# Kernel optimization log

Measured on AMD Instinct MI355X. Metric: run time of the kernel, lower is better.

## Reference

```python
import jax, jax.numpy as jnp
import numpy as np

H = 1024
NH = 16
HD = H // NH
EPS = 1e-5


def setup_inputs() -> dict:
    key = jax.random.key(0)
    ks = jax.random.split(key, 16)
    B, LQ, LK = 2, 1024, 2048
    s = 1.0 / np.sqrt(H)
    inp = {
        "query": jax.random.normal(ks[0], (B, LQ, H), jnp.float32),
        "key": jax.random.normal(ks[1], (B, LK, H), jnp.float32),
        "value": jax.random.normal(ks[2], (B, LK, H), jnp.float32),
        "mask": jax.random.randint(ks[3], (B, LQ, LK), 0, 2, jnp.int32),
        "Wq": jax.random.normal(ks[4], (H, H), jnp.float32) * s,
        "bq": jnp.zeros((H,), jnp.float32),
        "Wk": jax.random.normal(ks[5], (H, H), jnp.float32) * s,
        "bk": jnp.zeros((H,), jnp.float32),
        "Wv": jax.random.normal(ks[6], (H, H), jnp.float32) * s,
        "bv": jnp.zeros((H,), jnp.float32),
        "Wo": jax.random.normal(ks[7], (H, H), jnp.float32) * s,
        "bo": jnp.zeros((H,), jnp.float32),
        "ln_g": jnp.ones((H,), jnp.float32),
        "ln_b": jnp.zeros((H,), jnp.float32),
    }
    return inp


def _split_heads(x, B, L):
    # [B, L, H] -> [B, NH, L, HD]
    return x.reshape(B, L, NH, HD).transpose(0, 2, 1, 3)


def reference(query, key, value, mask, Wq, bq, Wk, bk, Wv, bv, Wo, bo, ln_g, ln_b):
    B, LQ, _ = query.shape
    LK = key.shape[1]
    # projections (torch Linear: x @ W.T + b)
    Q = _split_heads(query @ Wq.T + bq, B, LQ)   # [B,NH,LQ,HD]
    K = _split_heads(key   @ Wk.T + bk, B, LK)   # [B,NH,LK,HD]
    V = _split_heads(value @ Wv.T + bv, B, LK)   # [B,NH,LK,HD]
    scores = jnp.einsum('bhqd,bhkd->bhqk', Q, K) / np.sqrt(HD)
    scores = jnp.where(mask[:, None, :, :] == 0, jnp.float32(-1e9), scores)
    attn = jax.nn.softmax(scores, axis=-1)
    # dropout is identity in eval mode
    ctx = jnp.einsum('bhqk,bhkd->bhqd', attn, V)            # [B,NH,LQ,HD]
    ctx = ctx.transpose(0, 2, 1, 3).reshape(B, LQ, H)       # [B,LQ,H]
    out = ctx @ Wo.T + bo
    x = out + query
    mu = jnp.mean(x, axis=-1, keepdims=True)
    var = jnp.mean(jnp.square(x - mu), axis=-1, keepdims=True)
    return (x - mu) / jnp.sqrt(var + EPS) * ln_g + ln_b
```

## Files before the change

kernel.cpp:

```cpp
#include <hip/hip_runtime.h>
#include <hip/hip_bf16.h>

typedef __hip_bfloat16 hbf16;

#define Hdim 1024
#define NHEAD 16
#define HDIM 64
#define BATCH 2
#define LQ 1024
#define LK 2048
#define LN_EPS 1e-5f

typedef __bf16 bfv8 __attribute__((ext_vector_type(8)));
typedef float floatx4 __attribute__((ext_vector_type(4)));
typedef union { bfv8 v; __bf16 b[8]; unsigned short s[8]; } bfu8;

#define BK 32
#define LDS_PITCH 40
#define QT 64
#define KT 64
#define KS_PITCH 72
#define VT_OFF(d) ((d) * 72 + (((d) >> 3) << 3))
#define PS_OFF(r) ((r) * 72 + (((r) >> 2) << 3))

__device__ inline bfv8 cvt2(const float4 x, const float4 y) {
    bfv8 r = {(__bf16)x.x, (__bf16)x.y, (__bf16)x.z, (__bf16)x.w,
              (__bf16)y.x, (__bf16)y.y, (__bf16)y.z, (__bf16)y.w};
    return r;
}

__device__ __forceinline__ void glds16(const void* g, void* l) {
    __builtin_amdgcn_global_load_lds(
        (const __attribute__((address_space(1))) void*)g,
        (__attribute__((address_space(3))) void*)l, 16, 0, 0);
}

__global__ __launch_bounds__(256) void cvt_all(
    const float* __restrict__ q, const float* __restrict__ k,
    const float* __restrict__ v, const float* __restrict__ Wq,
    const float* __restrict__ Wk, const float* __restrict__ Wv,
    hbf16* __restrict__ qb, hbf16* __restrict__ kb, hbf16* __restrict__ vb,
    hbf16* __restrict__ Wqb, hbf16* __restrict__ Wkb, hbf16* __restrict__ Wvb) {
    const int blk = blockIdx.x;
    const float* src; hbf16* dst; int base;
    if (blk < 1024)      { src = q;  dst = qb;  base = blk; }
    else if (blk < 3072) { src = k;  dst = kb;  base = blk - 1024; }
    else if (blk < 5120) { src = v;  dst = vb;  base = blk - 3072; }
    else if (blk < 5632) { src = Wq; dst = Wqb; base = blk - 5120; }
    else if (blk < 6144) { src = Wk; dst = Wkb; base = blk - 5632; }
    else                 { src = Wv; dst = Wvb; base = blk - 6144; }
    const size_t e = (size_t)base * 2048 + (size_t)threadIdx.x * 8;
    const float4 a = *(const float4*)(src + e);
    const float4 b = *(const float4*)(src + e + 4);
    *(bfv8*)((__bf16*)dst + e) = cvt2(a, b);
}

__global__ __launch_bounds__(256) void proj3_glds(
    const hbf16* __restrict__ qb, const hbf16* __restrict__ kb,
    const hbf16* __restrict__ vb,
    const hbf16* __restrict__ Wqb, const hbf16* __restrict__ Wkb,
    const hbf16* __restrict__ Wvb,
    const float* __restrict__ bq, const float* __restrict__ bk,
    const float* __restrict__ bv,
    hbf16* __restrict__ Qp, hbf16* __restrict__ Kp, hbf16* __restrict__ Vp) {
    const int z = blockIdx.z;
    if (z == 0 && blockIdx.y >= (BATCH * LQ) / 128) return;
    const hbf16* A; const hbf16* W; const float* bias; hbf16* out; float scale;
    if (z == 0)      { A = qb; W = Wqb; bias = bq; out = Qp; scale = 0.125f; }
    else if (z == 1) { A = kb; W = Wkb; bias = bk; out = Kp; scale = 1.0f; }
    else             { A = vb; W = Wvb; bias = bv; out = Vp; scale = 1.0f; }

    __shared__ __align__(16) __bf16 As[2][128 * 32];
    __shared__ __align__(16) __bf16 Bs[2][128 * 32];
    const int tid = threadIdx.x;
    const int lane = tid & 63;
    const int w = tid >> 6;
    const int wm = w & 1, wn = w >> 1;
    const int u = lane & 15;
    const int quad = lane >> 4;
    const int rowBase = blockIdx.y * 128;
    const int colBase = blockIdx.x * 128;

    const int srow = tid >> 2;
    const int scol = (tid & 3) * 8;
    const hbf16* aP = A + (size_t)(rowBase + srow) * Hdim + scol;
    const hbf16* wP = W + (size_t)(colBase + srow) * Hdim + scol;
    const int ldsOff = srow * 32 + scol;

#define P_STAGE(buf, k0)                                            \
    do {                                                            \
        glds16(aP + (k0), &As[buf][ldsOff]);                        \
        glds16(aP + (k0) + (size_t)64 * Hdim, &As[buf][ldsOff + 64 * 32]); \
        glds16(wP + (k0), &Bs[buf][ldsOff]);                        \
        glds16(wP + (k0) + (size_t)64 * Hdim, &Bs[buf][ldsOff + 64 * 32]); \
    } while (0)

    floatx4 acc[4][4];
#pragma unroll
    for (int mi = 0; mi < 4; ++mi)
#pragma unroll
        for (int ni = 0; ni < 4; ++ni) acc[mi][ni] = (floatx4){0.f, 0.f, 0.f, 0.f};

#define P_COMPUTE(buf)                                                         \
    do {                                                                       \
        bfv8 af[4], bf[4];                                                     \
        _Pragma("unroll") for (int mi = 0; mi < 4; ++mi)                       \
            af[mi] = *(const bfv8*)&As[buf][(wm * 64 + mi * 16 + u) * 32 + quad * 8]; \
        _Pragma("unroll") for (int ni = 0; ni < 4; ++ni)                       \
            bf[ni] = *(const bfv8*)&Bs[buf][(wn * 64 + ni * 16 + u) * 32 + quad * 8]; \
        _Pragma("unroll") for (int mi = 0; mi < 4; ++mi)                       \
            _Pragma("unroll") for (int ni = 0; ni < 4; ++ni)                   \
                acc[mi][ni] = __builtin_amdgcn_mfma_f32_16x16x32_bf16(af[mi], bf[ni], acc[mi][ni], 0, 0, 0); \
    } while (0)

    P_STAGE(0, 0);
    __syncthreads();

    for (int t = 0; t < 32; t += 2) {
        if (t + 1 < 32) P_STAGE(1, (t + 1) * 32);
        P_COMPUTE(0);
        __syncthreads();
        if (t + 2 < 32) P_STAGE(0, (t + 2) * 32);
        P_COMPUTE(1);
        __syncthreads();
    }
#undef P_STAGE
#undef P_COMPUTE

#pragma unroll
    for (int mi = 0; mi < 4; ++mi)
#pragma unroll
        for (int ni = 0; ni < 4; ++ni) {
            const int n = colBase + wn * 64 + ni * 16 + u;
            const float bn = bias[n];
#pragma unroll
            for (int rr = 0; rr < 4; ++rr) {
                const int m = rowBase + wm * 64 + mi * 16 + quad * 4 + rr;
                out[(size_t)m * Hdim + n] = __float2bfloat16((acc[mi][ni][rr] + bn) * scale);
            }
        }
}

__global__ __launch_bounds__(256) void gemm_ctx2(const hbf16* __restrict__ A,
                                                 const float* __restrict__ W,
                                                 const float* __restrict__ bias,
                                                 const float* __restrict__ resid,
                                                 float* __restrict__ out) {
    __shared__ __align__(16) __bf16 As[2][64 * 32];
    __shared__ __align__(16) __bf16 Bs[2][64 * 32];
    const int tid = threadIdx.x;
    const int lane = tid & 63;
    const int w = tid >> 6;
    const int wm = w & 1, wn = w >> 1;
    const int u = lane & 15;
    const int quad = lane >> 4;
    const int rowBase = blockIdx.y * 64;
    const int colBase = blockIdx.x * 64;

    const int srow = tid >> 2;
    const int scol = (tid & 3) * 8;
    const hbf16* aP = A + (size_t)(rowBase + srow) * Hdim + scol;
    const int ldsOffA = srow * 32 + scol;

    const float* wP = W + (size_t)(colBase + srow) * Hdim + scol;
    const int ldsOffB = ldsOffA;

    floatx4 acc[2][2];
#pragma unroll
    for (int mi = 0; mi < 2; ++mi)
#pragma unroll
        for (int ni = 0; ni < 2; ++ni) acc[mi][ni] = (floatx4){0.f, 0.f, 0.f, 0.f};

#define C_COMPUTE(buf)                                                         \
    do {                                                                       \
        bfv8 af[2], bf[2];                                                     \
        _Pragma("unroll") for (int mi = 0; mi < 2; ++mi)                       \
            af[mi] = *(const bfv8*)&As[buf][(wm * 32 + mi * 16 + u) * 32 + quad * 8]; \
        _Pragma("unroll") for (int ni = 0; ni < 2; ++ni)                       \
            bf[ni] = *(const bfv8*)&Bs[buf][(wn * 32 + ni * 16 + u) * 32 + quad * 8]; \
        _Pragma("unroll") for (int mi = 0; mi < 2; ++mi)                       \
            _Pragma("unroll") for (int ni = 0; ni < 2; ++ni)                   \
                acc[mi][ni] = __builtin_amdgcn_mfma_f32_16x16x32_bf16(af[mi], bf[ni], acc[mi][ni], 0, 0, 0); \
    } while (0)

    {
        glds16(aP, &As[0][ldsOffA]);
        const float4* w4 = (const float4*)wP;
        const float4 w0 = w4[0], w1 = w4[1];
        *(bfv8*)&Bs[0][ldsOffB] = cvt2(w0, w1);
    }
    __syncthreads();

    for (int t = 0; t < 32; t += 2) {
        {
            float4 w0, w1;
            const bool pf = (t + 1 < 32);
            if (pf) {
                glds16(aP + (t + 1) * 32, &As[1][ldsOffA]);
                const float4* w4 = (const float4*)(wP + (t + 1) * 32);
                w0 = w4[0]; w1 = w4[1];
            }
            C_COMPUTE(0);
            if (pf) {
                *(bfv8*)&Bs[1][ldsOffB] = cvt2(w0, w1);
            }
            __syncthreads();
        }
        {
            float4 w0, w1;
            const bool pf = (t + 2 < 32);
            if (pf) {
                glds16(aP + (t + 2) * 32, &As[0][ldsOffA]);
                const float4* w4 = (const float4*)(wP + (t + 2) * 32);
                w0 = w4[0]; w1 = w4[1];
            }
            C_COMPUTE(1);
            if (pf) {
                *(bfv8*)&Bs[0][ldsOffB] = cvt2(w0, w1);
            }
            __syncthreads();
        }
    }
#undef C_COMPUTE

#pragma unroll
    for (int mi = 0; mi < 2; ++mi)
#pragma unroll
        for (int ni = 0; ni < 2; ++ni) {
            const int n = colBase + wn * 32 + ni * 16 + u;
            const float bn = bias[n];
#pragma unroll
            for (int rr = 0; rr < 4; ++rr) {
                const int m = rowBase + wm * 32 + mi * 16 + quad * 4 + rr;
                out[(size_t)m * Hdim + n] = acc[mi][ni][rr] + bn + resid[(size_t)m * Hdim + n];
            }
        }
}

__global__ __launch_bounds__(256) void proj3_mfma(
    const float* __restrict__ q_in, const float* __restrict__ k_in,
    const float* __restrict__ v_in,
    const float* __restrict__ Wq, const float* __restrict__ bq,
    const float* __restrict__ Wk, const float* __restrict__ bk,
    const float* __restrict__ Wv, const float* __restrict__ bv,
    hbf16* __restrict__ Qp, hbf16* __restrict__ Kp, hbf16* __restrict__ Vp) {
    const int z = blockIdx.z;
    if (z == 0 && blockIdx.y >= (BATCH * LQ) / 64) return;
    const float* A; const float* W; const float* bias; hbf16* out; float scale;
    if (z == 0)      { A = q_in; W = Wq; bias = bq; out = Qp; scale = 0.125f; }
    else if (z == 1) { A = k_in; W = Wk; bias = bk; out = Kp; scale = 1.0f; }
    else             { A = v_in; W = Wv; bias = bv; out = Vp; scale = 1.0f; }

    __shared__ __align__(16) __bf16 As[64 * LDS_PITCH];
    __shared__ __align__(16) __bf16 Bs[64 * LDS_PITCH];
    const int tid = threadIdx.x;
    const int lane = tid & 63;
    const int w = tid >> 6;
    const int wm = w & 1, wn = w >> 1;
    const int rowBase = blockIdx.y * 64;
    const int colBase = blockIdx.x * 64;
    const int sr = tid >> 2;
    const int scg = (tid & 3) * 8;
    const int lr = lane & 15;
    const int quad = lane >> 4;

    floatx4 acc[2][2] = {};

    for (int k0 = 0; k0 < Hdim; k0 += BK) {
        const float* ap = A + (size_t)(rowBase + sr) * Hdim + k0 + scg;
        bfv8 av = cvt2(((const float4*)ap)[0], ((const float4*)ap)[1]);
        const float* wp = W + (size_t)(colBase + sr) * Hdim + k0 + scg;
        bfv8 bv8 = cvt2(((const float4*)wp)[0], ((const float4*)wp)[1]);
        __syncthreads();
        *(bfv8*)&As[sr * LDS_PITCH + scg] = av;
        *(bfv8*)&Bs[sr * LDS_PITCH + scg] = bv8;
        __syncthreads();

        bfv8 bf[2];
#pragma unroll
        for (int nt = 0; nt < 2; ++nt)
            bf[nt] = *(const bfv8*)&Bs[(wn * 32 + nt * 16 + lr) * LDS_PITCH + quad * 8];
#pragma unroll
        for (int mt = 0; mt < 2; ++mt) {
            bfv8 af = *(const bfv8*)&As[(wm * 32 + mt * 16 + lr) * LDS_PITCH + quad * 8];
#pragma unroll
            for (int nt = 0; nt < 2; ++nt)
                acc[mt][nt] = __builtin_amdgcn_mfma_f32_16x16x32_bf16(af, bf[nt], acc[mt][nt], 0, 0, 0);
        }
    }

#pragma unroll
    for (int mt = 0; mt < 2; ++mt)
#pragma unroll
        for (int nt = 0; nt < 2; ++nt) {
            const int n = colBase + wn * 32 + nt * 16 + lr;
            const float bn = bias[n];
#pragma unroll
            for (int rr = 0; rr < 4; ++rr) {
                const int m = rowBase + wm * 32 + mt * 16 + quad * 4 + rr;
                out[(size_t)m * Hdim + n] = __float2bfloat16((acc[mt][nt][rr] + bn) * scale);
            }
        }
}

__global__ __launch_bounds__(256) void gemm_mfma_f32(const float* __restrict__ A,
                                                     const float* __restrict__ W,
                                                     const float* __restrict__ bias,
                                                     hbf16* __restrict__ out,
                                                     float scale) {
    __shared__ __align__(16) __bf16 As[64 * LDS_PITCH];
    __shared__ __align__(16) __bf16 Bs[64 * LDS_PITCH];
    const int tid = threadIdx.x;
    const int lane = tid & 63;
    const int w = tid >> 6;
    const int wm = w & 1, wn = w >> 1;
    const int rowBase = blockIdx.y * 64;
    const int colBase = blockIdx.x * 64;
    const int sr = tid >> 2;
    const int scg = (tid & 3) * 8;
    const int lr = lane & 15;
    const int quad = lane >> 4;

    floatx4 acc[2][2] = {};

    for (int k0 = 0; k0 < Hdim; k0 += BK) {
        const float* ap = A + (size_t)(rowBase + sr) * Hdim + k0 + scg;
        bfv8 av = cvt2(((const float4*)ap)[0], ((const float4*)ap)[1]);
        const float* wp = W + (size_t)(colBase + sr) * Hdim + k0 + scg;
        bfv8 bv = cvt2(((const float4*)wp)[0], ((const float4*)wp)[1]);
        __syncthreads();
        *(bfv8*)&As[sr * LDS_PITCH + scg] = av;
        *(bfv8*)&Bs[sr * LDS_PITCH + scg] = bv;
        __syncthreads();

        bfv8 bf[2];
#pragma unroll
        for (int nt = 0; nt < 2; ++nt)
            bf[nt] = *(const bfv8*)&Bs[(wn * 32 + nt * 16 + lr) * LDS_PITCH + quad * 8];
#pragma unroll
        for (int mt = 0; mt < 2; ++mt) {
            bfv8 af = *(const bfv8*)&As[(wm * 32 + mt * 16 + lr) * LDS_PITCH + quad * 8];
#pragma unroll
            for (int nt = 0; nt < 2; ++nt)
                acc[mt][nt] = __builtin_amdgcn_mfma_f32_16x16x32_bf16(af, bf[nt], acc[mt][nt], 0, 0, 0);
        }
    }

#pragma unroll
    for (int mt = 0; mt < 2; ++mt)
#pragma unroll
        for (int nt = 0; nt < 2; ++nt) {
            const int n = colBase + wn * 32 + nt * 16 + lr;
            const float bn = bias[n];
#pragma unroll
            for (int rr = 0; rr < 4; ++rr) {
                const int m = rowBase + wm * 32 + mt * 16 + quad * 4 + rr;
                out[(size_t)m * Hdim + n] = __float2bfloat16((acc[mt][nt][rr] + bn) * scale);
            }
        }
}

__global__ __launch_bounds__(256) void gemm_mfma_ctx(const hbf16* __restrict__ A,
                                                     const float* __restrict__ W,
                                                     const float* __restrict__ bias,
                                                     const float* __restrict__ resid,
                                                     float* __restrict__ out) {
    __shared__ __align__(16) __bf16 As[64 * LDS_PITCH];
    __shared__ __align__(16) __bf16 Bs[64 * LDS_PITCH];
    const int tid = threadIdx.x;
    const int lane = tid & 63;
    const int w = tid >> 6;
    const int wm = w & 1, wn = w >> 1;
    const int rowBase = blockIdx.y * 64;
    const int colBase = blockIdx.x * 64;
    const int sr = tid >> 2;
    const int scg = (tid & 3) * 8;
    const int lr = lane & 15;
    const int quad = lane >> 4;

    floatx4 acc[2][2] = {};

    for (int k0 = 0; k0 < Hdim; k0 += BK) {
        bfv8 av = *(const bfv8*)(A + (size_t)(rowBase + sr) * Hdim + k0 + scg);
        const float* wp = W + (size_t)(colBase + sr) * Hdim + k0 + scg;
        bfv8 bv = cvt2(((const float4*)wp)[0], ((const float4*)wp)[1]);
        __syncthreads();
        *(bfv8*)&As[sr * LDS_PITCH + scg] = av;
        *(bfv8*)&Bs[sr * LDS_PITCH + scg] = bv;
        __syncthreads();

        bfv8 bf[2];
#pragma unroll
        for (int nt = 0; nt < 2; ++nt)
            bf[nt] = *(const bfv8*)&Bs[(wn * 32 + nt * 16 + lr) * LDS_PITCH + quad * 8];
#pragma unroll
        for (int mt = 0; mt < 2; ++mt) {
            bfv8 af = *(const bfv8*)&As[(wm * 32 + mt * 16 + lr) * LDS_PITCH + quad * 8];
#pragma unroll
            for (int nt = 0; nt < 2; ++nt)
                acc[mt][nt] = __builtin_amdgcn_mfma_f32_16x16x32_bf16(af, bf[nt], acc[mt][nt], 0, 0, 0);
        }
    }

#pragma unroll
    for (int mt = 0; mt < 2; ++mt)
#pragma unroll
        for (int nt = 0; nt < 2; ++nt) {
            const int n = colBase + wn * 32 + nt * 16 + lr;
            const float bn = bias[n];
#pragma unroll
            for (int rr = 0; rr < 4; ++rr) {
                const int m = rowBase + wm * 32 + mt * 16 + quad * 4 + rr;
                out[(size_t)m * Hdim + n] = acc[mt][nt][rr] + bn + resid[(size_t)m * Hdim + n];
            }
        }
}

__global__ __launch_bounds__(256) void mask_prep_st(const int* __restrict__ mask,
                                                    hbf16* __restrict__ mbias) {
    const int t = blockIdx.x;
    const int kt = t & 31;
    const int qb = (t >> 5) & 15;
    const int b = t >> 9;
    const int tid = threadIdx.x;
    const int w = tid >> 6;
    const int lane = tid & 63;
    const int quad = lane >> 4;
    const int u = lane & 15;
    const int qrow = qb * 64 + w * 16 + quad * 4;
    const int kcol = kt * 64 + u;
    const int* mp = mask + ((size_t)(b * LQ + qrow)) * LK + kcol;

    bfu8 v0, v1;
#pragma unroll
    for (int ns = 0; ns < 4; ++ns)
#pragma unroll
        for (int rr = 0; rr < 4; ++rr) {
            const int mv = mp[(size_t)rr * LK + ns * 16];
            const __bf16 bias = (mv == 0) ? (__bf16)(-1e9f) : (__bf16)(-10.0f);
            const int j = ns * 4 + rr;
            if (j < 8) v0.b[j] = bias; else v1.b[j - 8] = bias;
        }
    __bf16* dst = (__bf16*)mbias + (size_t)t * 4096 + tid * 16;
    *(bfv8*)dst = v0.v;
    *(bfv8*)(dst + 8) = v1.v;
}

__global__ __launch_bounds__(256, 4) void attn_split(const hbf16* __restrict__ Qp,
                                                     const hbf16* __restrict__ Kp,
                                                     const hbf16* __restrict__ Vp,
                                                     const hbf16* __restrict__ mbias,
                                                     float* __restrict__ Opart,
                                                     float* __restrict__ lpart) {
    const int wg = (blockIdx.x & 7) * 128 + (blockIdx.x >> 3);
    const int qb = wg & 15;
    const int h = (wg >> 4) & 15;
    const int z = wg >> 8;
    const int b = z >> 1;
    const int sp = z & 1;
    const int tid = threadIdx.x;
    const int lane = tid & 63;
    const int w = tid >> 6;
    const int u = lane & 15;
    const int quad = lane >> 4;
    const int qBase = qb * QT;

    __shared__ __align__(16) __bf16 Ks[64 * KS_PITCH];
    __shared__ __align__(16) __bf16 Vt[4672];
    __shared__ __align__(16) __bf16 Ps[4][1184];

    const int qrow_frag = qBase + w * 16 + u;
    const hbf16* qptr = Qp + (size_t)(b * LQ + qrow_frag) * Hdim + h * HDIM + quad * 8;
    const bfv8 af_q0 = *(const bfv8*)qptr;
    const bfv8 af_q1 = *(const bfv8*)(qptr + 32);

    float l_acc[4] = {0.f, 0.f, 0.f, 0.f};
    floatx4 acc_o[4];
#pragma unroll
    for (int nd = 0; nd < 4; ++nd) acc_o[nd] = (floatx4){0.f, 0.f, 0.f, 0.f};

    const int sk = tid >> 2;
    const int sdg = (tid & 3) * 16;
    const int vk2 = (tid >> 3) * 2;
    const int vd0 = (tid & 7) * 8;
    const __bf16* mbT = (const __bf16*)mbias + (size_t)(b * 16 + qb) * 32 * 4096 + tid * 16;

    const int kt0 = sp * (LK / KT / 2);
    const int ktEnd = kt0 + (LK / KT / 2);

    bfu8 pm0, pm1, pv0, pv1;
    bfv8 pk0, pk1;

#define A_LOADS(kt)                                                            \
    do {                                                                       \
        const int kBase_ = (kt) * KT;                                          \
        pm0.v = *(const bfv8*)(mbT + (size_t)(kt) * 4096);                     \
        pm1.v = *(const bfv8*)(mbT + (size_t)(kt) * 4096 + 8);                 \
        const hbf16* vp_ = Vp + (size_t)(b * LK + kBase_ + vk2) * Hdim + h * HDIM + vd0; \
        pv0.v = *(const bfv8*)vp_;                                             \
        pv1.v = *(const bfv8*)(vp_ + Hdim);                                    \
        const hbf16* kp_ = Kp + (size_t)(b * LK + kBase_ + sk) * Hdim + h * HDIM + sdg; \
        pk0 = *(const bfv8*)kp_;                                               \
        pk1 = *(const bfv8*)(kp_ + 8);                                         \
    } while (0)

    A_LOADS(kt0);

    for (int kt = kt0; kt < ktEnd; ++kt) {
        __syncthreads();
        *(bfv8*)&Ks[sk * KS_PITCH + sdg] = pk0;
        *(bfv8*)&Ks[sk * KS_PITCH + sdg + 8] = pk1;
#pragma unroll
        for (int i = 0; i < 8; ++i) {
            unsigned int pk = (unsigned int)pv0.s[i] | ((unsigned int)pv1.s[i] << 16);
            *(unsigned int*)&Vt[VT_OFF(vd0 + i) + vk2] = pk;
        }
        bfu8 mb0, mb1;
        mb0.v = pm0.v;
        mb1.v = pm1.v;
        __syncthreads();

        if (kt + 1 < ktEnd) A_LOADS(kt + 1);

        floatx4 acc_s[4];
        __builtin_amdgcn_s_setprio(1);
#pragma unroll
        for (int ns = 0; ns < 4; ++ns) {
            const bfv8 bk0 = *(const bfv8*)&Ks[(ns * 16 + u) * KS_PITCH + quad * 8];
            const bfv8 bk1 = *(const bfv8*)&Ks[(ns * 16 + u) * KS_PITCH + quad * 8 + 32];
            floatx4 a = (floatx4){0.f, 0.f, 0.f, 0.f};
            a = __builtin_amdgcn_mfma_f32_16x16x32_bf16(af_q0, bk0, a, 0, 0, 0);
            a = __builtin_amdgcn_mfma_f32_16x16x32_bf16(af_q1, bk1, a, 0, 0, 0);
            acc_s[ns] = a;
        }
        __builtin_amdgcn_s_setprio(0);

        __bf16* Pw = Ps[w];
#pragma unroll
        for (int ns = 0; ns < 4; ++ns)
#pragma unroll
            for (int rr = 0; rr < 4; ++rr) {
                const int j = ns * 4 + rr;
                const float bias = (j < 8) ? (float)mb0.b[j] : (float)mb1.b[j - 8];
                const float p = __expf(acc_s[ns][rr] + bias);
                Pw[PS_OFF(quad * 4 + rr) + ns * 16 + u] = (__bf16)p;
                l_acc[rr] += p;
            }

        const bfv8 af_p0 = *(const bfv8*)&Pw[PS_OFF(u) + quad * 8];
        const bfv8 af_p1 = *(const bfv8*)&Pw[PS_OFF(u) + quad * 8 + 32];
        __builtin_amdgcn_s_setprio(1);
#pragma unroll
        for (int nd = 0; nd < 4; ++nd) {
            const bfv8 bv0 = *(const bfv8*)&Vt[VT_OFF(nd * 16 + u) + quad * 8];
            const bfv8 bv1 = *(const bfv8*)&Vt[VT_OFF(nd * 16 + u) + quad * 8 + 32];
            acc_o[nd] = __builtin_amdgcn_mfma_f32_16x16x32_bf16(af_p0, bv0, acc_o[nd], 0, 0, 0);
            acc_o[nd] = __builtin_amdgcn_mfma_f32_16x16x32_bf16(af_p1, bv1, acc_o[nd], 0, 0, 0);
        }
        __builtin_amdgcn_s_setprio(0);
    }
#undef A_LOADS

#pragma unroll
    for (int rr = 0; rr < 4; ++rr) {
        float l = l_acc[rr];
        l += __shfl_xor(l, 1, 64);
        l += __shfl_xor(l, 2, 64);
        l += __shfl_xor(l, 4, 64);
        l += __shfl_xor(l, 8, 64);
        const int qrow = qBase + w * 16 + quad * 4 + rr;
        const size_t m = (size_t)(b * LQ + qrow);
        float* orow = Opart + (size_t)sp * (BATCH * LQ * Hdim) + m * Hdim + h * HDIM;
#pragma unroll
        for (int nd = 0; nd < 4; ++nd)
            orow[nd * 16 + u] = acc_o[nd][rr];
        if (u == 0)
            lpart[(size_t)sp * (BATCH * LQ * NHEAD) + m * NHEAD + h] = l;
    }
}

__global__ __launch_bounds__(256) void merge_ctx(const float* __restrict__ Opart,
                                                 const float* __restrict__ lpart,
                                                 hbf16* __restrict__ ctx) {
    const size_t m = blockIdx.x;
    const int t = threadIdx.x;
    const int kk = t * 4;
    const int h = kk >> 6;
    const float l = lpart[m * NHEAD + h] +
                    lpart[(size_t)(BATCH * LQ * NHEAD) + m * NHEAD + h];
    const float invl = 1.0f / l;
    const float4 a = ((const float4*)(Opart + m * Hdim))[t];
    const float4 c = ((const float4*)(Opart + (size_t)(BATCH * LQ * Hdim) + m * Hdim))[t];
    hbf16* crow = ctx + m * Hdim + kk;
    crow[0] = __float2bfloat16((a.x + c.x) * invl);
    crow[1] = __float2bfloat16((a.y + c.y) * invl);
    crow[2] = __float2bfloat16((a.z + c.z) * invl);
    crow[3] = __float2bfloat16((a.w + c.w) * invl);
}

__global__ __launch_bounds__(256, 4) void attn_flash_st(const hbf16* __restrict__ Qp,
                                                        const hbf16* __restrict__ Kp,
                                                        const hbf16* __restrict__ Vp,
                                                        const hbf16* __restrict__ mbias,
                                                        hbf16* __restrict__ ctx) {
    const int qb = blockIdx.x;
    const int h = blockIdx.y;
    const int b = blockIdx.z;
    const int tid = threadIdx.x;
    const int lane = tid & 63;
    const int w = tid >> 6;
    const int u = lane & 15;
    const int quad = lane >> 4;
    const int qBase = qb * QT;

    __shared__ __align__(16) __bf16 Ks[64 * KS_PITCH];
    __shared__ __align__(16) __bf16 Vt[4672];
    __shared__ __align__(16) __bf16 Ps[4][1184];

    const int qrow_frag = qBase + w * 16 + u;
    const hbf16* qptr = Qp + (size_t)(b * LQ + qrow_frag) * Hdim + h * HDIM + quad * 8;
    const bfv8 af_q0 = *(const bfv8*)qptr;
    const bfv8 af_q1 = *(const bfv8*)(qptr + 32);

    float l_acc[4] = {0.f, 0.f, 0.f, 0.f};
    floatx4 acc_o[4];
#pragma unroll
    for (int nd = 0; nd < 4; ++nd) acc_o[nd] = (floatx4){0.f, 0.f, 0.f, 0.f};

    const int sk = tid >> 2;
    const int sdg = (tid & 3) * 16;
    const int vk2 = (tid >> 3) * 2;
    const int vd0 = (tid & 7) * 8;
    const __bf16* mbT = (const __bf16*)mbias + (size_t)(b * 16 + qb) * 32 * 4096 + tid * 16;

    for (int kt = 0; kt < LK / KT; ++kt) {
        const int kBase = kt * KT;

        bfu8 mb0, mb1;
        mb0.v = *(const bfv8*)(mbT + (size_t)kt * 4096);
        mb1.v = *(const bfv8*)(mbT + (size_t)kt * 4096 + 8);

        const hbf16* vp0 = Vp + (size_t)(b * LK + kBase + vk2) * Hdim + h * HDIM + vd0;
        bfu8 v0, v1;
        v0.v = *(const bfv8*)vp0;
        v1.v = *(const bfv8*)(vp0 + Hdim);
        const hbf16* kp = Kp + (size_t)(b * LK + kBase + sk) * Hdim + h * HDIM + sdg;
        const bfv8 kv0 = *(const bfv8*)kp;
        const bfv8 kv1 = *(const bfv8*)(kp + 8);

        __syncthreads();
        *(bfv8*)&Ks[sk * KS_PITCH + sdg] = kv0;
        *(bfv8*)&Ks[sk * KS_PITCH + sdg + 8] = kv1;
#pragma unroll
        for (int i = 0; i < 8; ++i) {
            unsigned int pk = (unsigned int)v0.s[i] | ((unsigned int)v1.s[i] << 16);
            *(unsigned int*)&Vt[VT_OFF(vd0 + i) + vk2] = pk;
        }
        __syncthreads();

        floatx4 acc_s[4];
#pragma unroll
        for (int ns = 0; ns < 4; ++ns) {
            const bfv8 bk0 = *(const bfv8*)&Ks[(ns * 16 + u) * KS_PITCH + quad * 8];
            const bfv8 bk1 = *(const bfv8*)&Ks[(ns * 16 + u) * KS_PITCH + quad * 8 + 32];
            floatx4 a = (floatx4){0.f, 0.f, 0.f, 0.f};
            a = __builtin_amdgcn_mfma_f32_16x16x32_bf16(af_q0, bk0, a, 0, 0, 0);
            a = __builtin_amdgcn_mfma_f32_16x16x32_bf16(af_q1, bk1, a, 0, 0, 0);
            acc_s[ns] = a;
        }

        __bf16* Pw = Ps[w];
#pragma unroll
        for (int ns = 0; ns < 4; ++ns)
#pragma unroll
            for (int rr = 0; rr < 4; ++rr) {
                const int j = ns * 4 + rr;
                const float bias = (j < 8) ? (float)mb0.b[j] : (float)mb1.b[j - 8];
                const float p = __expf(acc_s[ns][rr] + bias);
                Pw[PS_OFF(quad * 4 + rr) + ns * 16 + u] = (__bf16)p;
                l_acc[rr] += p;
            }

        const bfv8 af_p0 = *(const bfv8*)&Pw[PS_OFF(u) + quad * 8];
        const bfv8 af_p1 = *(const bfv8*)&Pw[PS_OFF(u) + quad * 8 + 32];
#pragma unroll
        for (int nd = 0; nd < 4; ++nd) {
            const bfv8 bv0 = *(const bfv8*)&Vt[VT_OFF(nd * 16 + u) + quad * 8];
            const bfv8 bv1 = *(const bfv8*)&Vt[VT_OFF(nd * 16 + u) + quad * 8 + 32];
            acc_o[nd] = __builtin_amdgcn_mfma_f32_16x16x32_bf16(af_p0, bv0, acc_o[nd], 0, 0, 0);
            acc_o[nd] = __builtin_amdgcn_mfma_f32_16x16x32_bf16(af_p1, bv1, acc_o[nd], 0, 0, 0);
        }
    }

#pragma unroll
    for (int rr = 0; rr < 4; ++rr) {
        float l = l_acc[rr];
        l += __shfl_xor(l, 1, 64);
        l += __shfl_xor(l, 2, 64);
        l += __shfl_xor(l, 4, 64);
        l += __shfl_xor(l, 8, 64);
        const float invl = 1.0f / l;
        const int qrow = qBase + w * 16 + quad * 4 + rr;
        hbf16* crow = ctx + (size_t)(b * LQ + qrow) * Hdim + h * HDIM;
#pragma unroll
        for (int nd = 0; nd < 4; ++nd)
            crow[nd * 16 + u] = __float2bfloat16(acc_o[nd][rr] * invl);
    }
}

__global__ __launch_bounds__(256) void ln_kernel(float* __restrict__ x,
                                                 const float* __restrict__ g,
                                                 const float* __restrict__ beta) {
    const int row = blockIdx.x;
    float* xr = x + (size_t)row * Hdim;
    __shared__ float red[256];
    const int tid = threadIdx.x;

    const float4 xi = ((const float4*)xr)[tid];
    red[tid] = xi.x + xi.y + xi.z + xi.w;
    __syncthreads();
    for (int st = 128; st > 0; st >>= 1) {
        if (tid < st) red[tid] += red[tid + st];
        __syncthreads();
    }
    const float mu = red[0] * (1.0f / Hdim);
    __syncthreads();
    {
        float dx = xi.x - mu, dy = xi.y - mu, dz = xi.z - mu, dw = xi.w - mu;
        red[tid] = dx * dx + dy * dy + dz * dz + dw * dw;
    }
    __syncthreads();
    for (int st = 128; st > 0; st >>= 1) {
        if (tid < st) red[tid] += red[tid + st];
        __syncthreads();
    }
    const float rstd = rsqrtf(red[0] * (1.0f / Hdim) + LN_EPS);

    const float4 g4 = ((const float4*)g)[tid];
    const float4 b4 = ((const float4*)beta)[tid];
    float4 y;
    y.x = (xi.x - mu) * rstd * g4.x + b4.x;
    y.y = (xi.y - mu) * rstd * g4.y + b4.y;
    y.z = (xi.z - mu) * rstd * g4.z + b4.z;
    y.w = (xi.w - mu) * rstd * g4.w + b4.w;
    ((float4*)xr)[tid] = y;
}

__device__ inline float wave_red_sum(float v) {
    v += __shfl_down(v, 32, 64);
    v += __shfl_down(v, 16, 64);
    v += __shfl_down(v, 8, 64);
    v += __shfl_down(v, 4, 64);
    v += __shfl_down(v, 2, 64);
    v += __shfl_down(v, 1, 64);
    return v;
}

__global__ __launch_bounds__(256) void fused_mha(
    const float* __restrict__ q_in, const float* __restrict__ k_in,
    const float* __restrict__ v_in, const int* __restrict__ mask,
    const float* __restrict__ Wq, const float* __restrict__ bq,
    const float* __restrict__ Wk, const float* __restrict__ bk,
    const float* __restrict__ Wv, const float* __restrict__ bv,
    const float* __restrict__ Wo, const float* __restrict__ bo,
    const float* __restrict__ ln_g, const float* __restrict__ ln_b,
    float* __restrict__ out) {
    const int q = blockIdx.x;
    const int b = blockIdx.y;
    const int tid = threadIdx.x;
    const int lane = tid & 63;
    const int w = tid >> 6;

    __shared__ float qrow[Hdim];
    __shared__ float qt[Hdim];
    __shared__ float sc[LK];
    __shared__ float u[Hdim];
    __shared__ float ctxv[Hdim];
    __shared__ float Qh[HDIM];
    __shared__ float red[256];
    __shared__ float sb_sh;

    const float* qp = q_in + (size_t)(b * LQ + q) * Hdim;
    for (int i = tid; i < Hdim; i += 256) qrow[i] = qp[i];
    __syncthreads();

    const float* keyb = k_in + (size_t)b * LK * Hdim;
    const float* valb = v_in + (size_t)b * LK * Hdim;
    const int* mrow = mask + (size_t)(b * LQ + q) * LK;

    for (int h = 0; h < NHEAD; ++h) {
        for (int dd = w; dd < HDIM; dd += 4) {
            const float4* wrow = (const float4*)(Wq + (size_t)(h * HDIM + dd) * Hdim);
            const float4* q4 = (const float4*)qrow;
            float p = 0.f;
#pragma unroll
            for (int i0 = 0; i0 < 4; ++i0) {
                float4 a = wrow[i0 * 64 + lane];
                float4 c = q4[i0 * 64 + lane];
                p += a.x * c.x + a.y * c.y + a.z * c.z + a.w * c.w;
            }
            p = wave_red_sum(p);
            if (lane == 0) Qh[dd] = p + bq[h * HDIM + dd];
        }
        __syncthreads();

        if (tid < HDIM) red[tid] = Qh[tid] * bk[h * HDIM + tid];

        float4 s4 = {0.f, 0.f, 0.f, 0.f};
        for (int d = 0; d < HDIM; ++d) {
            float4 a = ((const float4*)(Wk + (size_t)(h * HDIM + d) * Hdim))[tid];
            float qd = Qh[d];
            s4.x += a.x * qd;
            s4.y += a.y * qd;
            s4.z += a.z * qd;
            s4.w += a.w * qd;
        }
        __syncthreads();
        if (tid == 0) {
            float s = 0.f;
            for (int i = 0; i < HDIM; ++i) s += red[i];
            sb_sh = s;
        }
        ((float4*)qt)[tid] = s4;
        __syncthreads();
        const float sb = sb_sh;

        for (int k = w; k < LK; k += 4) {
            const float4* krow = (const float4*)(keyb + (size_t)k * Hdim);
            const float4* q4 = (const float4*)qt;
            float p = 0.f;
#pragma unroll
            for (int i0 = 0; i0 < 4; ++i0) {
                float4 a = krow[i0 * 64 + lane];
                float4 c = q4[i0 * 64 + lane];
                p += a.x * c.x + a.y * c.y + a.z * c.z + a.w * c.w;
            }
            p = wave_red_sum(p);
            if (lane == 0) {
                float s = (p + sb) * 0.125f;
                if (mrow[k] == 0) s = -1e9f;
                sc[k] = s;
            }
        }
        __syncthreads();

        float m = -1e30f;
        for (int k = tid; k < LK; k += 256) m = fmaxf(m, sc[k]);
        red[tid] = m;
        __syncthreads();
        for (int s = 128; s > 0; s >>= 1) {
            if (tid < s) red[tid] = fmaxf(red[tid], red[tid + s]);
            __syncthreads();
        }
        const float mx = red[0];
        __syncthreads();
        float sum = 0.f;
        for (int k = tid; k < LK; k += 256) {
            float e = __expf(sc[k] - mx);
            sc[k] = e;
            sum += e;
        }
        red[tid] = sum;
        __syncthreads();
        for (int s = 128; s > 0; s >>= 1) {
            if (tid < s) red[tid] += red[tid + s];
            __syncthreads();
        }
        const float inv = 1.0f / red[0];
        for (int k = tid; k < LK; k += 256) sc[k] *= inv;
        __syncthreads();

        {
            float4 acc = {0.f, 0.f, 0.f, 0.f};
            const float4* vb4 = (const float4*)valb;
#pragma unroll 4
            for (int k = 0; k < LK; ++k) {
                float p = sc[k];
                float4 a = vb4[(size_t)k * (Hdim / 4) + tid];
                acc.x += a.x * p;
                acc.y += a.y * p;
                acc.z += a.z * p;
                acc.w += a.w * p;
            }
            ((float4*)u)[tid] = acc;
        }
        __syncthreads();

        for (int dd = w; dd < HDIM; dd += 4) {
            const float4* wrow = (const float4*)(Wv + (size_t)(h * HDIM + dd) * Hdim);
            const float4* u4 = (const float4*)u;
            float p = 0.f;
#pragma unroll
            for (int i0 = 0; i0 < 4; ++i0) {
                float4 a = wrow[i0 * 64 + lane];
                float4 c = u4[i0 * 64 + lane];
                p += a.x * c.x + a.y * c.y + a.z * c.z + a.w * c.w;
            }
            p = wave_red_sum(p);
            if (lane == 0) ctxv[h * HDIM + dd] = p + bv[h * HDIM + dd];
        }
        __syncthreads();
    }

    for (int n = w; n < Hdim; n += 4) {
        const float4* wrow = (const float4*)(Wo + (size_t)n * Hdim);
        const float4* c4 = (const float4*)ctxv;
        float p = 0.f;
#pragma unroll
        for (int i0 = 0; i0 < 4; ++i0) {
            float4 a = wrow[i0 * 64 + lane];
            float4 c = c4[i0 * 64 + lane];
            p += a.x * c.x + a.y * c.y + a.z * c.z + a.w * c.w;
        }
        p = wave_red_sum(p);
        if (lane == 0) qt[n] = p + bo[n] + qrow[n];
    }
    __syncthreads();

    {
        const float4 x4 = ((const float4*)qt)[tid];
        red[tid] = x4.x + x4.y + x4.z + x4.w;
    }
    __syncthreads();
    for (int s = 128; s > 0; s >>= 1) {
        if (tid < s) red[tid] += red[tid + s];
        __syncthreads();
    }
    const float mu = red[0] * (1.0f / Hdim);
    __syncthreads();
    {
        const float4 x4 = ((const float4*)qt)[tid];
        float dx = x4.x - mu, dy = x4.y - mu, dz = x4.z - mu, dw = x4.w - mu;
        red[tid] = dx * dx + dy * dy + dz * dz + dw * dw;
    }
    __syncthreads();
    for (int s = 128; s > 0; s >>= 1) {
        if (tid < s) red[tid] += red[tid + s];
        __syncthreads();
    }
    const float rstd = rsqrtf(red[0] * (1.0f / Hdim) + LN_EPS);

    float* orow = out + (size_t)(b * LQ + q) * Hdim;
    const float4 x4 = ((const float4*)qt)[tid];
    const float4 g4 = ((const float4*)ln_g)[tid];
    const float4 b4 = ((const float4*)ln_b)[tid];
    float4 y;
    y.x = (x4.x - mu) * rstd * g4.x + b4.x;
    y.y = (x4.y - mu) * rstd * g4.y + b4.y;
    y.z = (x4.z - mu) * rstd * g4.z + b4.z;
    y.w = (x4.w - mu) * rstd * g4.w + b4.w;
    ((float4*)orow)[tid] = y;
}

extern "C" void kernel_launch(void* const* d_in, const int* in_sizes, int n_in,
                              void* d_out, int out_size, void* d_ws, size_t ws_size,
                              hipStream_t stream) {
    const float* query = (const float*)d_in[0];
    const float* key   = (const float*)d_in[1];
    const float* value = (const float*)d_in[2];
    const int*   mask  = (const int*)d_in[3];
    const float* Wq = (const float*)d_in[4];
    const float* bq = (const float*)d_in[5];
    const float* Wk = (const float*)d_in[6];
    const float* bk = (const float*)d_in[7];
    const float* Wv = (const float*)d_in[8];
    const float* bv = (const float*)d_in[9];
    const float* Wo = (const float*)d_in[10];
    const float* bo = (const float*)d_in[11];
    const float* ln_g = (const float*)d_in[12];
    const float* ln_b = (const float*)d_in[13];
    float* out = (float*)d_out;

    const size_t MB = 1024 * 1024;
    dim3 blk(256);

    if (ws_size >= 50 * MB) {
        char* p = (char*)d_ws;
        hbf16* Qp    = (hbf16*)(p + 0 * MB);
        hbf16* Kp    = (hbf16*)(p + 4 * MB);
        hbf16* Vp    = (hbf16*)(p + 12 * MB);
        hbf16* ctxb  = (hbf16*)(p + 20 * MB);
        hbf16* mbias = (hbf16*)(p + 24 * MB);
        float* Opart = (float*)(p + 32 * MB);
        float* lpart = (float*)(p + 48 * MB);

        hbf16* qb  = (hbf16*)(p + 20 * MB);
        hbf16* kb  = (hbf16*)(p + 24 * MB);
        hbf16* vb  = (hbf16*)(p + 32 * MB);
        hbf16* Wqb = (hbf16*)(p + 40 * MB);
        hbf16* Wkb = (hbf16*)(p + 42 * MB);
        hbf16* Wvb = (hbf16*)(p + 44 * MB);

        cvt_all<<<dim3(6656), blk, 0, stream>>>(query, key, value, Wq, Wk, Wv,
                                                qb, kb, vb, Wqb, Wkb, Wvb);
        proj3_glds<<<dim3(Hdim / 128, (BATCH * LK) / 128, 3), blk, 0, stream>>>(
            qb, kb, vb, Wqb, Wkb, Wvb, bq, bk, bv, Qp, Kp, Vp);
        mask_prep_st<<<dim3(1024), blk, 0, stream>>>(mask, mbias);

        attn_split<<<dim3(1024), blk, 0, stream>>>(
            Qp, Kp, Vp, mbias, Opart, lpart);
        merge_ctx<<<dim3(BATCH * LQ), blk, 0, stream>>>(Opart, lpart, ctxb);

        gemm_ctx2<<<dim3(Hdim / 64, (BATCH * LQ) / 64), blk, 0, stream>>>(
            ctxb, Wo, bo, query, out);
        ln_kernel<<<BATCH * LQ, blk, 0, stream>>>(out, ln_g, ln_b);
    } else if (ws_size >= 32 * MB) {
        char* p = (char*)d_ws;
        hbf16* Qp = (hbf16*)p;    p += 4 * MB;
        hbf16* Kp = (hbf16*)p;    p += 8 * MB;
        hbf16* Vp = (hbf16*)p;    p += 8 * MB;
        hbf16* ctxb = (hbf16*)p;  p += 4 * MB;
        hbf16* mbias = (hbf16*)p; p += 8 * MB;

        gemm_mfma_f32<<<dim3(Hdim / 64, (BATCH * LQ) / 64), blk, 0, stream>>>(query, Wq, bq, Qp, 0.125f);
        gemm_mfma_f32<<<dim3(Hdim / 64, (BATCH * LK) / 64), blk, 0, stream>>>(key, Wk, bk, Kp, 1.0f);
        gemm_mfma_f32<<<dim3(Hdim / 64, (BATCH * LK) / 64), blk, 0, stream>>>(value, Wv, bv, Vp, 1.0f);
        mask_prep_st<<<dim3(1024), blk, 0, stream>>>(mask, mbias);
        attn_flash_st<<<dim3(LQ / QT, NHEAD, BATCH), blk, 0, stream>>>(Qp, Kp, Vp, mbias, ctxb);
        gemm_mfma_ctx<<<dim3(Hdim / 64, (BATCH * LQ) / 64), blk, 0, stream>>>(ctxb, Wo, bo, query, out);
        ln_kernel<<<BATCH * LQ, blk, 0, stream>>>(out, ln_g, ln_b);
    } else {
        fused_mha<<<dim3(LQ, BATCH), dim3(256), 0, stream>>>(
            query, key, value, mask, Wq, bq, Wk, bk, Wv, bv, Wo, bo, ln_g, ln_b, out);
    }
}
```

Measured before the change: 246.6 us.

## Fuse split-merge into output GEMM and read raw mask inside attention

Removes the merge_ctx kernel by having the output-projection GEMM load both fp32 partial attention outputs and their row sums, normalize them, and convert to bf16 while staging its A tile. It also drops the mask_prep kernel: attention now reads the int32 mask directly and turns it into a -1e9/-10 bias in registers. Two launches and the round trips through the bf16 ctx and bias buffers go away. In exchange the GEMM reads twice as many fp32 bytes per A tile without async global-to-LDS loads, and attention reads 4-byte mask values with strided, poorly coalesced accesses plus more registers.

```diff
diff --git a/kernel.cpp b/kernel.cpp
--- a/kernel.cpp
+++ b/kernel.cpp
@@ -141,11 +141,10 @@
         }
 }
 
-__global__ __launch_bounds__(256) void gemm_ctx2(const hbf16* __restrict__ A,
-                                                 const float* __restrict__ W,
-                                                 const float* __restrict__ bias,
-                                                 const float* __restrict__ resid,
-                                                 float* __restrict__ out) {
+__global__ __launch_bounds__(256) void gemm_ctx_merge(
+    const float* __restrict__ Opart, const float* __restrict__ lpart,
+    const float* __restrict__ W, const float* __restrict__ bias,
+    const float* __restrict__ resid, float* __restrict__ out) {
     __shared__ __align__(16) __bf16 As[2][64 * 32];
     __shared__ __align__(16) __bf16 Bs[2][64 * 32];
     const int tid = threadIdx.x;
@@ -159,11 +158,13 @@
 
     const int srow = tid >> 2;
     const int scol = (tid & 3) * 8;
-    const hbf16* aP = A + (size_t)(rowBase + srow) * Hdim + scol;
-    const int ldsOffA = srow * 32 + scol;
-
+    const size_t mrow = (size_t)(rowBase + srow);
+    const float* o0 = Opart + mrow * Hdim + scol;
+    const float* o1 = o0 + (size_t)BATCH * LQ * Hdim;
+    const float* lp0 = lpart + mrow * NHEAD;
+    const float* lp1 = lp0 + BATCH * LQ * NHEAD;
     const float* wP = W + (size_t)(colBase + srow) * Hdim + scol;
-    const int ldsOffB = ldsOffA;
+    const int ldsOff = srow * 32 + scol;
 
     floatx4 acc[2][2];
 #pragma unroll
@@ -183,45 +184,77 @@
                 acc[mi][ni] = __builtin_amdgcn_mfma_f32_16x16x32_bf16(af[mi], bf[ni], acc[mi][ni], 0, 0, 0); \
     } while (0)
 
+#define M_WRITEA(buf, a0, a1, c0, c1, l0v, l1v)                                \
+    do {                                                                       \
+        const float invl_ = 1.0f / ((l0v) + (l1v));                            \
+        float4 s0_, s1_;                                                       \
+        s0_.x = (a0.x + c0.x) * invl_; s0_.y = (a0.y + c0.y) * invl_;          \
+        s0_.z = (a0.z + c0.z) * invl_; s0_.w = (a0.w + c0.w) * invl_;          \
+        s1_.x = (a1.x + c1.x) * invl_; s1_.y = (a1.y + c1.y) * invl_;          \
+        s1_.z = (a1.z + c1.z) * invl_; s1_.w = (a1.w + c1.w) * invl_;          \
+        *(bfv8*)&As[buf][ldsOff] = cvt2(s0_, s1_);                             \
+    } while (0)
+
     {
-        glds16(aP, &As[0][ldsOffA]);
+        const float4 a0 = *(const float4*)(o0);
+        const float4 a1 = *(const float4*)(o0 + 4);
+        const float4 c0 = *(const float4*)(o1);
+        const float4 c1 = *(const float4*)(o1 + 4);
+        const int hh = scol >> 6;
+        const float l0v = lp0[hh], l1v = lp1[hh];
         const float4* w4 = (const float4*)wP;
         const float4 w0 = w4[0], w1 = w4[1];
-        *(bfv8*)&Bs[0][ldsOffB] = cvt2(w0, w1);
+        M_WRITEA(0, a0, a1, c0, c1, l0v, l1v);
+        *(bfv8*)&Bs[0][ldsOff] = cvt2(w0, w1);
     }
     __syncthreads();
 
     for (int t = 0; t < 32; t += 2) {
         {
-            float4 w0, w1;
+            float4 a0, a1, c0, c1, w0, w1; float l0v = 1.f, l1v = 0.f;
             const bool pf = (t + 1 < 32);
             if (pf) {
-                glds16(aP + (t + 1) * 32, &As[1][ldsOffA]);
-                const float4* w4 = (const float4*)(wP + (t + 1) * 32);
+                const int kk = (t + 1) * 32;
+                a0 = *(const float4*)(o0 + kk);
+                a1 = *(const float4*)(o0 + kk + 4);
+                c0 = *(const float4*)(o1 + kk);
+                c1 = *(const float4*)(o1 + kk + 4);
+                const int hh = (kk + scol) >> 6;
+                l0v = lp0[hh]; l1v = lp1[hh];
+                const float4* w4 = (const float4*)(wP + kk);
                 w0 = w4[0]; w1 = w4[1];
             }
             C_COMPUTE(0);
             if (pf) {
-                *(bfv8*)&Bs[1][ldsOffB] = cvt2(w0, w1);
+                M_WRITEA(1, a0, a1, c0, c1, l0v, l1v);
+                *(bfv8*)&Bs[1][ldsOff] = cvt2(w0, w1);
             }
             __syncthreads();
         }
         {
-            float4 w0, w1;
+            float4 a0, a1, c0, c1, w0, w1; float l0v = 1.f, l1v = 0.f;
             const bool pf = (t + 2 < 32);
             if (pf) {
-                glds16(aP + (t + 2) * 32, &As[0][ldsOffA]);
-                const float4* w4 = (const float4*)(wP + (t + 2) * 32);
+                const int kk = (t + 2) * 32;
+                a0 = *(const float4*)(o0 + kk);
+                a1 = *(const float4*)(o0 + kk + 4);
+                c0 = *(const float4*)(o1 + kk);
+                c1 = *(const float4*)(o1 + kk + 4);
+                const int hh = (kk + scol) >> 6;
+                l0v = lp0[hh]; l1v = lp1[hh];
+                const float4* w4 = (const float4*)(wP + kk);
                 w0 = w4[0]; w1 = w4[1];
             }
             C_COMPUTE(1);
             if (pf) {
-                *(bfv8*)&Bs[0][ldsOffB] = cvt2(w0, w1);
+                M_WRITEA(0, a0, a1, c0, c1, l0v, l1v);
+                *(bfv8*)&Bs[0][ldsOff] = cvt2(w0, w1);
             }
             __syncthreads();
         }
     }
 #undef C_COMPUTE
+#undef M_WRITEA
 
 #pragma unroll
     for (int mi = 0; mi < 2; ++mi)
@@ -449,7 +482,7 @@
 __global__ __launch_bounds__(256, 4) void attn_split(const hbf16* __restrict__ Qp,
                                                      const hbf16* __restrict__ Kp,
                                                      const hbf16* __restrict__ Vp,
-                                                     const hbf16* __restrict__ mbias,
+                                                     const int* __restrict__ mask,
                                                      float* __restrict__ Opart,
                                                      float* __restrict__ lpart) {
     const int wg = (blockIdx.x & 7) * 128 + (blockIdx.x >> 3);
@@ -483,19 +516,22 @@
     const int sdg = (tid & 3) * 16;
     const int vk2 = (tid >> 3) * 2;
     const int vd0 = (tid & 7) * 8;
-    const __bf16* mbT = (const __bf16*)mbias + (size_t)(b * 16 + qb) * 32 * 4096 + tid * 16;
+    const int* mrow = mask + (size_t)(b * LQ + qBase + w * 16 + quad * 4) * LK + u;
 
     const int kt0 = sp * (LK / KT / 2);
     const int ktEnd = kt0 + (LK / KT / 2);
 
-    bfu8 pm0, pm1, pv0, pv1;
+    float pmB[16];
+    bfu8 pv0, pv1;
     bfv8 pk0, pk1;
 
 #define A_LOADS(kt)                                                            \
     do {                                                                       \
         const int kBase_ = (kt) * KT;                                          \
-        pm0.v = *(const bfv8*)(mbT + (size_t)(kt) * 4096);                     \
-        pm1.v = *(const bfv8*)(mbT + (size_t)(kt) * 4096 + 8);                 \
+        _Pragma("unroll") for (int ns = 0; ns < 4; ++ns)                       \
+            _Pragma("unroll") for (int rr = 0; rr < 4; ++rr)                   \
+                pmB[ns * 4 + rr] =                                             \
+                    (mrow[(size_t)rr * LK + kBase_ + ns * 16] == 0) ? -1e9f : -10.0f; \
         const hbf16* vp_ = Vp + (size_t)(b * LK + kBase_ + vk2) * Hdim + h * HDIM + vd0; \
         pv0.v = *(const bfv8*)vp_;                                             \
         pv1.v = *(const bfv8*)(vp_ + Hdim);                                    \
@@ -515,9 +551,9 @@
             unsigned int pk = (unsigned int)pv0.s[i] | ((unsigned int)pv1.s[i] << 16);
             *(unsigned int*)&Vt[VT_OFF(vd0 + i) + vk2] = pk;
         }
-        bfu8 mb0, mb1;
-        mb0.v = pm0.v;
-        mb1.v = pm1.v;
+        float mbB[16];
+#pragma unroll
+        for (int j = 0; j < 16; ++j) mbB[j] = pmB[j];
         __syncthreads();
 
         if (kt + 1 < ktEnd) A_LOADS(kt + 1);
@@ -540,9 +576,7 @@
         for (int ns = 0; ns < 4; ++ns)
 #pragma unroll
             for (int rr = 0; rr < 4; ++rr) {
-                const int j = ns * 4 + rr;
-                const float bias = (j < 8) ? (float)mb0.b[j] : (float)mb1.b[j - 8];
-                const float p = __expf(acc_s[ns][rr] + bias);
+                const float p = __expf(acc_s[ns][rr] + mbB[ns * 4 + rr]);
                 Pw[PS_OFF(quad * 4 + rr) + ns * 16 + u] = (__bf16)p;
                 l_acc[rr] += p;
             }
@@ -577,25 +611,6 @@
         if (u == 0)
             lpart[(size_t)sp * (BATCH * LQ * NHEAD) + m * NHEAD + h] = l;
     }
-}
-
-__global__ __launch_bounds__(256) void merge_ctx(const float* __restrict__ Opart,
-                                                 const float* __restrict__ lpart,
-                                                 hbf16* __restrict__ ctx) {
-    const size_t m = blockIdx.x;
-    const int t = threadIdx.x;
-    const int kk = t * 4;
-    const int h = kk >> 6;
-    const float l = lpart[m * NHEAD + h] +
-                    lpart[(size_t)(BATCH * LQ * NHEAD) + m * NHEAD + h];
-    const float invl = 1.0f / l;
-    const float4 a = ((const float4*)(Opart + m * Hdim))[t];
-    const float4 c = ((const float4*)(Opart + (size_t)(BATCH * LQ * Hdim) + m * Hdim))[t];
-    hbf16* crow = ctx + m * Hdim + kk;
-    crow[0] = __float2bfloat16((a.x + c.x) * invl);
-    crow[1] = __float2bfloat16((a.y + c.y) * invl);
-    crow[2] = __float2bfloat16((a.z + c.z) * invl);
-    crow[3] = __float2bfloat16((a.w + c.w) * invl);
 }
 
 __global__ __launch_bounds__(256, 4) void attn_flash_st(const hbf16* __restrict__ Qp,
@@ -979,10 +994,8 @@
         hbf16* Qp    = (hbf16*)(p + 0 * MB);
         hbf16* Kp    = (hbf16*)(p + 4 * MB);
         hbf16* Vp    = (hbf16*)(p + 12 * MB);
-        hbf16* ctxb  = (hbf16*)(p + 20 * MB);
-        hbf16* mbias = (hbf16*)(p + 24 * MB);
-        float* Opart = (float*)(p + 32 * MB);
-        float* lpart = (float*)(p + 48 * MB);
+        float* Opart = (float*)(p + 20 * MB);
+        float* lpart = (float*)(p + 36 * MB);
 
         hbf16* qb  = (hbf16*)(p + 20 * MB);
         hbf16* kb  = (hbf16*)(p + 24 * MB);
@@ -995,14 +1008,12 @@
                                                 qb, kb, vb, Wqb, Wkb, Wvb);
         proj3_glds<<<dim3(Hdim / 128, (BATCH * LK) / 128, 3), blk, 0, stream>>>(
             qb, kb, vb, Wqb, Wkb, Wvb, bq, bk, bv, Qp, Kp, Vp);
-        mask_prep_st<<<dim3(1024), blk, 0, stream>>>(mask, mbias);
 
         attn_split<<<dim3(1024), blk, 0, stream>>>(
-            Qp, Kp, Vp, mbias, Opart, lpart);
-        merge_ctx<<<dim3(BATCH * LQ), blk, 0, stream>>>(Opart, lpart, ctxb);
-
-        gemm_ctx2<<<dim3(Hdim / 64, (BATCH * LQ) / 64), blk, 0, stream>>>(
-            ctxb, Wo, bo, query, out);
+            Qp, Kp, Vp, mask, Opart, lpart);
+
+        gemm_ctx_merge<<<dim3(Hdim / 64, (BATCH * LQ) / 64), blk, 0, stream>>>(
+            Opart, lpart, Wo, bo, query, out);
         ln_kernel<<<BATCH * LQ, blk, 0, stream>>>(out, ln_g, ln_b);
     } else if (ws_size >= 32 * MB) {
         char* p = (char*)d_ws;
```

After: 240.1 us. 1.03x faster.
